# Optimization experiments

Measured on AMD Instinct MI355X. Metric: run time of the kernel, lower is better.

Reference implementation:

```python
import jax, jax.numpy as jnp
import numpy as np

B, S, H = 32, 256, 128
K, C, DSUB, O = 8, 4096, 16, 6  # PQ subspaces, ncentroids=4096, subvector dim, bits/symbol


def setup_inputs() -> dict:
    key = jax.random.key(0)
    ks = jax.random.split(key, 8)
    return {
        "z": jax.random.normal(ks[0], (B, S, 3), jnp.float32),
        "W1": jax.random.normal(ks[1], (3, H), jnp.float32) * 0.3,
        "b1": jax.random.normal(ks[2], (H,), jnp.float32) * 0.1,
        "W2": jax.random.normal(ks[3], (H, H), jnp.float32) * 0.1,
        "b2": jax.random.normal(ks[4], (H,), jnp.float32) * 0.1,
        "centroids": jax.random.normal(ks[5], (K, C, DSUB), jnp.float32),
        "W3": jax.random.normal(ks[6], (H, O), jnp.float32) * 0.1,
        "b3": jax.random.normal(ks[7], (O,), jnp.float32) * 0.1,
    }


def reference(z, W1, b1, W2, b2, centroids, W3, b3):
    # Small demapper MLP (layers 1-2, exact dense math)
    h1 = jax.nn.relu(z @ W1 + b1)            # [B,S,H]
    h2 = jax.nn.relu(h1 @ W2 + b2)           # [B,S,H] == layer3in
    N = B * S
    x = h2.reshape(N, K, DSUB)               # split rows into K PQ subvectors
    # Encode: nearest centroid per subspace (||x-c||^2 argmin; ||x||^2 is constant per row)
    dots = jnp.einsum("nkd,kcd->nkc", x, centroids)      # [N,K,C]
    c_norm = jnp.sum(centroids * centroids, axis=-1)      # [K,C]
    codes = jnp.argmin(c_norm[None, :, :] - 2.0 * dots, axis=-1)  # [N,K] int
    # LUT: precomputed centroid @ W3 per subspace
    W3r = W3.reshape(K, DSUB, O)
    lut = jnp.einsum("kcd,kdo->kco", centroids, W3r)      # [K,C,O]
    # Approximate matmul: sum of LUT entries selected by codes
    approx = jnp.sum(lut[jnp.arange(K)[None, :], codes], axis=1)  # [N,O]
    llr = (approx + b3).reshape(B, S * O)                 # [B, n]
    return llr
```

## Files before the change

### kernel.cpp

```cpp
#include <hip/hip_runtime.h>
#include <stdint.h>

#define NROWS 8192
#define HDIM  128
#define KSUB  8
#define NC    4096
#define DSUB  16
#define OUTD  6

#define FB_TAU 4e-3f
#define DOTSCALE (-2.0f / 4096.0f)

typedef _Float16 f16x8 __attribute__((ext_vector_type(8)));
typedef float    f32x4 __attribute__((ext_vector_type(4)));

#define XK_OFF 0u
#define CN_OFF 4194304u
#define B1_OFF 4325376u
#define PK_OFF 6422528u
#define M2_OFF 7471104u
#define CO_OFF B1_OFF

__global__ __launch_bounds__(256) void bprep_kernel(
    const float* __restrict__ ce, f16x8* __restrict__ B1)
{
    const int e = blockIdx.x * 256 + threadIdx.x;
    const int k    = e >> 14;
    const int tile = (e >> 6) & 255;
    const int lane = e & 63;
    const int col  = lane & 15;
    const int quad = lane >> 4;
    const int dims = (quad & 1) * 8;
    const int part = quad >> 1;
    const int n = tile * 16 + col;
    const float* cp = &ce[((size_t)k * NC + n) * DSUB + dims];
    f16x8 hi, lo;
    #pragma unroll
    for (int j = 0; j < 8; ++j) {
        const float s = cp[j] * 16.0f;
        const _Float16 h = (_Float16)s;
        hi[j] = h;
        lo[j] = (_Float16)(s - (float)h);
    }
    B1[e] = part ? lo : hi;
}

__global__ __launch_bounds__(256) void mlp_kernel(
    const float* __restrict__ z, const float* __restrict__ W1, const float* __restrict__ b1,
    const float* __restrict__ W2, const float* __restrict__ b2,
    const float* __restrict__ centroids,
    float* __restrict__ xk, float* __restrict__ cnorm)
{
    __shared__ float h1s[32 * HDIM];
    __shared__ float w2s[HDIM * HDIM];
    const int t = threadIdx.x;
    const int row0 = blockIdx.x * 32;

    if (blockIdx.x < (KSUB * NC) / 256) {
        const int g = blockIdx.x * 256 + t;
        const float4* cp = (const float4*)&centroids[(size_t)g * DSUB];
        float nn = 0.f;
        #pragma unroll
        for (int q = 0; q < 4; ++q) {
            const float4 v = cp[q];
            nn = fmaf(v.x, v.x, nn); nn = fmaf(v.y, v.y, nn);
            nn = fmaf(v.z, v.z, nn); nn = fmaf(v.w, v.w, nn);
        }
        cnorm[g] = nn;
    }

    {
        const float4* g4 = (const float4*)W2;
        float4* s4 = (float4*)w2s;
        #pragma unroll
        for (int q = 0; q < 16; ++q) s4[t + q * 256] = g4[t + q * 256];
    }

    #pragma unroll
    for (int e = 0; e < 16; ++e) {
        const int idx = e * 256 + t;
        const int r = idx >> 7, j = idx & 127;
        const int n = row0 + r;
        float acc = b1[j];
        acc = fmaf(z[n * 3 + 0], W1[0 * HDIM + j], acc);
        acc = fmaf(z[n * 3 + 1], W1[1 * HDIM + j], acc);
        acc = fmaf(z[n * 3 + 2], W1[2 * HDIM + j], acc);
        h1s[idx] = fmaxf(acc, 0.f);
    }
    __syncthreads();

    const int c4 = (t & 31) * 4;
    const int r4 = (t >> 5) * 4;
    float acc[4][4];
    #pragma unroll
    for (int a = 0; a < 4; ++a)
        #pragma unroll
        for (int b = 0; b < 4; ++b) acc[a][b] = 0.f;

    for (int k4 = 0; k4 < HDIM; k4 += 4) {
        float hh[4][4], ww[4][4];
        #pragma unroll
        for (int q = 0; q < 4; ++q) {
            const float4 v = *(const float4*)&h1s[(r4 + q) * HDIM + k4];
            hh[q][0] = v.x; hh[q][1] = v.y; hh[q][2] = v.z; hh[q][3] = v.w;
        }
        #pragma unroll
        for (int p = 0; p < 4; ++p) {
            const float4 v = *(const float4*)&w2s[(k4 + p) * HDIM + c4];
            ww[p][0] = v.x; ww[p][1] = v.y; ww[p][2] = v.z; ww[p][3] = v.w;
        }
        #pragma unroll
        for (int q = 0; q < 4; ++q)
            #pragma unroll
            for (int p = 0; p < 4; ++p) {
                acc[q][0] = fmaf(hh[q][p], ww[p][0], acc[q][0]);
                acc[q][1] = fmaf(hh[q][p], ww[p][1], acc[q][1]);
                acc[q][2] = fmaf(hh[q][p], ww[p][2], acc[q][2]);
                acc[q][3] = fmaf(hh[q][p], ww[p][3], acc[q][3]);
            }
    }

    const float4 bb = *(const float4*)&b2[c4];
    const int kk = c4 >> 4;
    const int dd = c4 & 15;
    #pragma unroll
    for (int q = 0; q < 4; ++q) {
        float4 o;
        o.x = fmaxf(acc[q][0] + bb.x, 0.f);
        o.y = fmaxf(acc[q][1] + bb.y, 0.f);
        o.z = fmaxf(acc[q][2] + bb.z, 0.f);
        o.w = fmaxf(acc[q][3] + bb.w, 0.f);
        *(float4*)&xk[((size_t)kk * NROWS + (row0 + r4 + q)) * DSUB + dd] = o;
    }
}

__global__ __launch_bounds__(256, 4) void argmin_kernel(
    const float* __restrict__ xk, const f16x8* __restrict__ B1,
    const float* __restrict__ cnorm,
    unsigned long long* __restrict__ pk, float* __restrict__ m2s)
{
    const int t = threadIdx.x;
    const int lane = t & 63;
    const int wid  = t >> 6;
    const int k  = blockIdx.y;
    const int cz = blockIdx.z;
    const int rb = blockIdx.x * 4 + wid;
    const int col  = lane & 15;
    const int quad = lane >> 4;
    const int dims = (quad & 1) * 8;
    const int part = quad >> 1;
    const int ct0 = cz * 128;

    f16x8 A[2];
    #pragma unroll
    for (int g = 0; g < 2; ++g) {
        const int row = rb * 32 + g * 16 + col;
        const float* xp = &xk[((size_t)k * NROWS + row) * DSUB + dims];
        f16x8 hi, lo;
        #pragma unroll
        for (int j = 0; j < 8; ++j) {
            const float s = xp[j] * 256.0f;
            const _Float16 h = (_Float16)s;
            hi[j] = h;
            lo[j] = (_Float16)(s - (float)h);
        }
        A[g] = part ? lo : hi;
    }

    float m1[2][4], m2[2][4];
    int   idx[2][4];
    #pragma unroll
    for (int g = 0; g < 2; ++g)
        #pragma unroll
        for (int j = 0; j < 4; ++j) { m1[g][j] = 1e30f; m2[g][j] = 1e30f; idx[g][j] = 0; }

    const f16x8* bp = &B1[((size_t)k * 256 + ct0) * 64];
    const float* cnp = &cnorm[k * NC + ct0 * 16 + col];
    const int l2 = lane ^ 32;

    f16x8 cb1 = bp[lane], cb2 = bp[l2];
    float cnv = cnp[0];

    for (int tt = 0; tt < 128; ++tt) {
        const f16x8 b1 = cb1, b2 = cb2;
        const float nrm = cnv;
        if (tt + 1 < 128) {
            cb1 = bp[(tt + 1) * 64 + lane];
            cb2 = bp[(tt + 1) * 64 + l2];
            cnv = cnp[(tt + 1) * 16];
        }
        f32x4 z4 = {0.f, 0.f, 0.f, 0.f};
        f32x4 a0a = __builtin_amdgcn_mfma_f32_16x16x32_f16(A[0], b1, z4, 0, 0, 0);
        f32x4 a0b = __builtin_amdgcn_mfma_f32_16x16x32_f16(A[0], b2, z4, 0, 0, 0);
        f32x4 a1a = __builtin_amdgcn_mfma_f32_16x16x32_f16(A[1], b1, z4, 0, 0, 0);
        f32x4 a1b = __builtin_amdgcn_mfma_f32_16x16x32_f16(A[1], b2, z4, 0, 0, 0);
        const int c = (ct0 + tt) * 16 + col;
        #pragma unroll
        for (int j = 0; j < 4; ++j) {
            {
                const float s = fmaf(a0a[j] + a0b[j], DOTSCALE, nrm);
                const bool lt = s < m1[0][j];
                m2[0][j] = __builtin_amdgcn_fmed3f(s, m1[0][j], m2[0][j]);
                idx[0][j] = lt ? c : idx[0][j];
                m1[0][j] = fminf(s, m1[0][j]);
            }
            {
                const float s = fmaf(a1a[j] + a1b[j], DOTSCALE, nrm);
                const bool lt = s < m1[1][j];
                m2[1][j] = __builtin_amdgcn_fmed3f(s, m1[1][j], m2[1][j]);
                idx[1][j] = lt ? c : idx[1][j];
                m1[1][j] = fminf(s, m1[1][j]);
            }
        }
    }

    #pragma unroll
    for (int off = 1; off < 16; off <<= 1) {
        #pragma unroll
        for (int g = 0; g < 2; ++g)
            #pragma unroll
            for (int j = 0; j < 4; ++j) {
                const float om1 = __shfl_xor(m1[g][j], off, 64);
                const float om2 = __shfl_xor(m2[g][j], off, 64);
                const int  oidx = __shfl_xor(idx[g][j], off, 64);
                const bool better = (om1 < m1[g][j]) ||
                                    (om1 == m1[g][j] && oidx < idx[g][j]);
                m2[g][j] = fminf(fminf(m2[g][j], om2), fmaxf(m1[g][j], om1));
                m1[g][j] = better ? om1 : m1[g][j];
                idx[g][j] = better ? oidx : idx[g][j];
            }
    }

    if (col == 0) {
        #pragma unroll
        for (int g = 0; g < 2; ++g)
            #pragma unroll
            for (int j = 0; j < 4; ++j) {
                const int row = rb * 32 + g * 16 + quad * 4 + j;
                unsigned u = __float_as_uint(m1[g][j]);
                u = (u & 0x80000000u) ? ~u : (u | 0x80000000u);
                pk [((size_t)cz * NROWS + row) * KSUB + k] =
                    ((unsigned long long)u << 32) | (unsigned)idx[g][j];
                m2s[((size_t)cz * NROWS + row) * KSUB + k] = m2[g][j];
            }
    }
}

__global__ __launch_bounds__(256) void fallback_kernel(
    const float* __restrict__ xk, const float* __restrict__ ce,
    const float* __restrict__ cnorm, const unsigned long long* __restrict__ pk,
    const float* __restrict__ m2s, int* __restrict__ codes)
{
    const int wg = blockIdx.x * 4 + (threadIdx.x >> 6);
    const int lane = threadIdx.x & 63;

    const unsigned long long a = pk[wg];
    const unsigned long long b = pk[(size_t)NROWS * KSUB + wg];
    const unsigned long long w = a < b ? a : b;
    const unsigned long long l = a < b ? b : a;
    const unsigned uw = (unsigned)(w >> 32), ul = (unsigned)(l >> 32);
    const float m1  = __uint_as_float((uw & 0x80000000u) ? (uw ^ 0x80000000u) : ~uw);
    const float m1l = __uint_as_float((ul & 0x80000000u) ? (ul ^ 0x80000000u) : ~ul);
    const float m2 = fminf(fminf(m2s[wg], m2s[(size_t)NROWS * KSUB + wg]), m1l);

    if (m2 - m1 >= FB_TAU) {
        if (lane == 0) codes[wg] = (int)(w & 0xFFFFFFFFull);
        return;
    }

    const int row = wg >> 3, k = wg & 7;
    float xr[DSUB];
    {
        const float* xp = &xk[((size_t)k * NROWS + row) * DSUB];
        #pragma unroll
        for (int q = 0; q < DSUB; q += 4) {
            const float4 v = *(const float4*)&xp[q];
            xr[q + 0] = -2.f * v.x; xr[q + 1] = -2.f * v.y;
            xr[q + 2] = -2.f * v.z; xr[q + 3] = -2.f * v.w;
        }
    }
    float bm = 1e30f; int bi = NC;
    for (int c = lane; c < NC; c += 64) {
        const float* cp = &ce[((size_t)k * NC + c) * DSUB];
        float s = cnorm[k * NC + c];
        #pragma unroll
        for (int d = 0; d < DSUB; ++d) s = fmaf(xr[d], cp[d], s);
        if (s < bm) { bm = s; bi = c; }
    }
    #pragma unroll
    for (int off = 1; off < 64; off <<= 1) {
        const float om = __shfl_xor(bm, off, 64);
        const int  oi = __shfl_xor(bi, off, 64);
        const bool better = (om < bm) || (om == bm && oi < bi);
        bm = better ? om : bm;
        bi = better ? oi : bi;
    }
    if (lane == 0) codes[wg] = bi;
}

__global__ __launch_bounds__(256) void out_kernel(
    const float* __restrict__ centroids, const float* __restrict__ W3,
    const float* __restrict__ b3, const int* __restrict__ codes,
    float* __restrict__ out)
{
    const int gid = blockIdx.x * 256 + threadIdx.x;
    const int n = gid / OUTD;
    const int o = gid - n * OUTD;
    float acc = b3[o];
    #pragma unroll
    for (int k = 0; k < KSUB; ++k) {
        const int code = codes[n * KSUB + k];
        const float* cp = &centroids[((size_t)k * NC + code) * DSUB];
        const float* wp = &W3[(k * DSUB) * OUTD + o];
        #pragma unroll
        for (int d = 0; d < DSUB; ++d)
            acc = fmaf(cp[d], wp[d * OUTD], acc);
    }
    out[gid] = acc;
}

extern "C" void kernel_launch(void* const* d_in, const int* in_sizes, int n_in,
                              void* d_out, int out_size, void* d_ws, size_t ws_size,
                              hipStream_t stream)
{
    const float* z  = (const float*)d_in[0];
    const float* W1 = (const float*)d_in[1];
    const float* b1 = (const float*)d_in[2];
    const float* W2 = (const float*)d_in[3];
    const float* b2 = (const float*)d_in[4];
    const float* ce = (const float*)d_in[5];
    const float* W3 = (const float*)d_in[6];
    const float* b3 = (const float*)d_in[7];

    char* ws = (char*)d_ws;
    float* xk     = (float*)(ws + XK_OFF);
    float* cnorm  = (float*)(ws + CN_OFF);
    f16x8* B1     = (f16x8*)(ws + B1_OFF);
    unsigned long long* pk = (unsigned long long*)(ws + PK_OFF);
    float* m2s    = (float*)(ws + M2_OFF);
    int*   codes  = (int*)  (ws + CO_OFF);

    hipLaunchKernelGGL(bprep_kernel, dim3(512), dim3(256), 0, stream, ce, B1);
    hipLaunchKernelGGL(mlp_kernel, dim3(NROWS / 32), dim3(256), 0, stream,
                       z, W1, b1, W2, b2, ce, xk, cnorm);
    hipLaunchKernelGGL(argmin_kernel, dim3(64, 8, 2), dim3(256), 0, stream,
                       xk, B1, cnorm, pk, m2s);
    hipLaunchKernelGGL(fallback_kernel, dim3(NROWS * KSUB / 4), dim3(256), 0, stream,
                       xk, ce, cnorm, pk, m2s, codes);
    hipLaunchKernelGGL(out_kernel, dim3((NROWS * OUTD) / 256), dim3(256), 0, stream,
                       ce, W3, b3, codes, (float*)d_out);
}
```

Baseline: 194.7 us.

## Fuse prep kernels, stage centroids in LDS, split argmin 4-way, merge fallback with output

Folds the centroid split-prep into the MLP kernel and merges the fallback and output kernels into one finish kernel that compacts the rows needing exact fallback into a worklist. Five launches become three. The argmin now splits centroids four ways, stages centroid tiles in shared memory, chains the hi/lo MFMAs into one accumulator, and packs the margin to the second-best as fp16 into the pk word, which removes the separate m2s buffer. The goals are less launch overhead, better grid parallelism and fewer global passes. In exchange the fp16 margin loses precision, the code field is narrowed to 16 bits, and the new __syncthreads add overhead in the argmin loop.

```diff
diff --git a/kernel.cpp b/kernel.cpp
--- a/kernel.cpp
+++ b/kernel.cpp
@@ -1,4 +1,5 @@
 #include <hip/hip_runtime.h>
+#include <hip/hip_fp16.h>
 #include <stdint.h>
 
 #define NROWS 8192
@@ -18,47 +19,46 @@
 #define CN_OFF 4194304u
 #define B1_OFF 4325376u
 #define PK_OFF 6422528u
-#define M2_OFF 7471104u
-#define CO_OFF B1_OFF
-
-__global__ __launch_bounds__(256) void bprep_kernel(
-    const float* __restrict__ ce, f16x8* __restrict__ B1)
-{
-    const int e = blockIdx.x * 256 + threadIdx.x;
-    const int k    = e >> 14;
-    const int tile = (e >> 6) & 255;
-    const int lane = e & 63;
-    const int col  = lane & 15;
-    const int quad = lane >> 4;
-    const int dims = (quad & 1) * 8;
-    const int part = quad >> 1;
-    const int n = tile * 16 + col;
-    const float* cp = &ce[((size_t)k * NC + n) * DSUB + dims];
-    f16x8 hi, lo;
-    #pragma unroll
-    for (int j = 0; j < 8; ++j) {
-        const float s = cp[j] * 16.0f;
-        const _Float16 h = (_Float16)s;
-        hi[j] = h;
-        lo[j] = (_Float16)(s - (float)h);
-    }
-    B1[e] = part ? lo : hi;
-}
-
-__global__ __launch_bounds__(256) void mlp_kernel(
+
+__global__ __launch_bounds__(256) void prep_kernel(
     const float* __restrict__ z, const float* __restrict__ W1, const float* __restrict__ b1,
     const float* __restrict__ W2, const float* __restrict__ b2,
-    const float* __restrict__ centroids,
-    float* __restrict__ xk, float* __restrict__ cnorm)
+    const float* __restrict__ ce,
+    float* __restrict__ xk, float* __restrict__ cnorm, f16x8* __restrict__ B1S)
 {
     __shared__ float h1s[32 * HDIM];
     __shared__ float w2s[HDIM * HDIM];
     const int t = threadIdx.x;
-    const int row0 = blockIdx.x * 32;
-
-    if (blockIdx.x < (KSUB * NC) / 256) {
-        const int g = blockIdx.x * 256 + t;
-        const float4* cp = (const float4*)&centroids[(size_t)g * DSUB];
+
+    if (blockIdx.x < 512) {
+        const int e = blockIdx.x * 256 + t;
+        const int k    = e >> 14;
+        const int tile = (e >> 6) & 255;
+        const int lane = e & 63;
+        const int col  = lane & 15;
+        const int quad = lane >> 4;
+        const int dims = (quad & 1) * 8;
+        const int part = quad >> 1;
+        const int n = tile * 16 + col;
+        const float* cp = &ce[((size_t)k * NC + n) * DSUB + dims];
+        f16x8 hi, lo;
+        #pragma unroll
+        for (int j = 0; j < 8; ++j) {
+            const float s = cp[j] * 16.0f;
+            const _Float16 h = (_Float16)s;
+            hi[j] = h;
+            lo[j] = (_Float16)(s - (float)h);
+        }
+        B1S[e] = part ? lo : hi;
+        return;
+    }
+
+    const int bx = blockIdx.x - 512;
+    const int row0 = bx * 32;
+
+    if (bx < (KSUB * NC) / 256) {
+        const int g = bx * 256 + t;
+        const float4* cp = (const float4*)&ce[(size_t)g * DSUB];
         float nn = 0.f;
         #pragma unroll
         for (int q = 0; q < 4; ++q) {
@@ -135,10 +135,10 @@
 }
 
 __global__ __launch_bounds__(256, 4) void argmin_kernel(
-    const float* __restrict__ xk, const f16x8* __restrict__ B1,
-    const float* __restrict__ cnorm,
-    unsigned long long* __restrict__ pk, float* __restrict__ m2s)
+    const float* __restrict__ xk, const f16x8* __restrict__ B1S,
+    const float* __restrict__ cnorm, unsigned long long* __restrict__ pk)
 {
+    __shared__ f16x8 cs[16 * 64];
     const int t = threadIdx.x;
     const int lane = t & 63;
     const int wid  = t >> 6;
@@ -149,7 +149,6 @@
     const int quad = lane >> 4;
     const int dims = (quad & 1) * 8;
     const int part = quad >> 1;
-    const int ct0 = cz * 128;
 
     f16x8 A[2];
     #pragma unroll
@@ -174,42 +173,48 @@
         #pragma unroll
         for (int j = 0; j < 4; ++j) { m1[g][j] = 1e30f; m2[g][j] = 1e30f; idx[g][j] = 0; }
 
-    const f16x8* bp = &B1[((size_t)k * 256 + ct0) * 64];
-    const float* cnp = &cnorm[k * NC + ct0 * 16 + col];
-    const int l2 = lane ^ 32;
-
-    f16x8 cb1 = bp[lane], cb2 = bp[l2];
-    float cnv = cnp[0];
-
-    for (int tt = 0; tt < 128; ++tt) {
-        const f16x8 b1 = cb1, b2 = cb2;
-        const float nrm = cnv;
-        if (tt + 1 < 128) {
-            cb1 = bp[(tt + 1) * 64 + lane];
-            cb2 = bp[(tt + 1) * 64 + l2];
-            cnv = cnp[(tt + 1) * 16];
-        }
-        f32x4 z4 = {0.f, 0.f, 0.f, 0.f};
-        f32x4 a0a = __builtin_amdgcn_mfma_f32_16x16x32_f16(A[0], b1, z4, 0, 0, 0);
-        f32x4 a0b = __builtin_amdgcn_mfma_f32_16x16x32_f16(A[0], b2, z4, 0, 0, 0);
-        f32x4 a1a = __builtin_amdgcn_mfma_f32_16x16x32_f16(A[1], b1, z4, 0, 0, 0);
-        f32x4 a1b = __builtin_amdgcn_mfma_f32_16x16x32_f16(A[1], b2, z4, 0, 0, 0);
-        const int c = (ct0 + tt) * 16 + col;
-        #pragma unroll
-        for (int j = 0; j < 4; ++j) {
-            {
-                const float s = fmaf(a0a[j] + a0b[j], DOTSCALE, nrm);
-                const bool lt = s < m1[0][j];
-                m2[0][j] = __builtin_amdgcn_fmed3f(s, m1[0][j], m2[0][j]);
-                idx[0][j] = lt ? c : idx[0][j];
-                m1[0][j] = fminf(s, m1[0][j]);
-            }
-            {
-                const float s = fmaf(a1a[j] + a1b[j], DOTSCALE, nrm);
-                const bool lt = s < m1[1][j];
-                m2[1][j] = __builtin_amdgcn_fmed3f(s, m1[1][j], m2[1][j]);
-                idx[1][j] = lt ? c : idx[1][j];
-                m1[1][j] = fminf(s, m1[1][j]);
+    const f16x8* gp  = &B1S[((size_t)k * 256 + cz * 64) * 64];
+    const float* cnp = &cnorm[k * NC + cz * 64 * 16 + col];
+
+    for (int ch = 0; ch < 4; ++ch) {
+        __syncthreads();
+        {
+            const uint4* g4 = (const uint4*)(gp + (size_t)ch * 1024);
+            uint4* s4 = (uint4*)cs;
+            #pragma unroll
+            for (int q = 0; q < 4; ++q) s4[t + q * 256] = g4[t + q * 256];
+        }
+        float nr[16];
+        #pragma unroll
+        for (int tt = 0; tt < 16; ++tt) nr[tt] = cnp[(ch * 16 + tt) * 16];
+        __syncthreads();
+
+        #pragma unroll
+        for (int tt = 0; tt < 16; ++tt) {
+            const f16x8 b1 = cs[tt * 64 + lane];
+            const f16x8 b2 = cs[tt * 64 + (lane ^ 32)];
+            const f32x4 zz = {0.f, 0.f, 0.f, 0.f};
+            f32x4 p0 = __builtin_amdgcn_mfma_f32_16x16x32_f16(A[0], b1, zz, 0, 0, 0);
+            p0       = __builtin_amdgcn_mfma_f32_16x16x32_f16(A[0], b2, p0, 0, 0, 0);
+            f32x4 p1 = __builtin_amdgcn_mfma_f32_16x16x32_f16(A[1], b1, zz, 0, 0, 0);
+            p1       = __builtin_amdgcn_mfma_f32_16x16x32_f16(A[1], b2, p1, 0, 0, 0);
+            const int c = ((cz * 64 + ch * 16 + tt) << 4) + col;
+            #pragma unroll
+            for (int j = 0; j < 4; ++j) {
+                {
+                    const float s = fmaf(p0[j], DOTSCALE, nr[tt]);
+                    const bool lt = s < m1[0][j];
+                    m2[0][j] = __builtin_amdgcn_fmed3f(s, m1[0][j], m2[0][j]);
+                    idx[0][j] = lt ? c : idx[0][j];
+                    m1[0][j] = fminf(s, m1[0][j]);
+                }
+                {
+                    const float s = fmaf(p1[j], DOTSCALE, nr[tt]);
+                    const bool lt = s < m1[1][j];
+                    m2[1][j] = __builtin_amdgcn_fmed3f(s, m1[1][j], m2[1][j]);
+                    idx[1][j] = lt ? c : idx[1][j];
+                    m1[1][j] = fminf(s, m1[1][j]);
+                }
             }
         }
     }
@@ -239,84 +244,112 @@
                 const int row = rb * 32 + g * 16 + quad * 4 + j;
                 unsigned u = __float_as_uint(m1[g][j]);
                 u = (u & 0x80000000u) ? ~u : (u | 0x80000000u);
-                pk [((size_t)cz * NROWS + row) * KSUB + k] =
-                    ((unsigned long long)u << 32) | (unsigned)idx[g][j];
-                m2s[((size_t)cz * NROWS + row) * KSUB + k] = m2[g][j];
+                const unsigned short dh =
+                    __half_as_ushort(__float2half(m2[g][j] - m1[g][j]));
+                pk[((size_t)cz * NROWS + row) * KSUB + k] =
+                    ((unsigned long long)u << 32) |
+                    ((unsigned)dh << 16) | (unsigned)idx[g][j];
             }
     }
 }
 
-__global__ __launch_bounds__(256) void fallback_kernel(
+__global__ __launch_bounds__(256) void finish_kernel(
     const float* __restrict__ xk, const float* __restrict__ ce,
     const float* __restrict__ cnorm, const unsigned long long* __restrict__ pk,
-    const float* __restrict__ m2s, int* __restrict__ codes)
-{
-    const int wg = blockIdx.x * 4 + (threadIdx.x >> 6);
-    const int lane = threadIdx.x & 63;
-
-    const unsigned long long a = pk[wg];
-    const unsigned long long b = pk[(size_t)NROWS * KSUB + wg];
-    const unsigned long long w = a < b ? a : b;
-    const unsigned long long l = a < b ? b : a;
-    const unsigned uw = (unsigned)(w >> 32), ul = (unsigned)(l >> 32);
-    const float m1  = __uint_as_float((uw & 0x80000000u) ? (uw ^ 0x80000000u) : ~uw);
-    const float m1l = __uint_as_float((ul & 0x80000000u) ? (ul ^ 0x80000000u) : ~ul);
-    const float m2 = fminf(fminf(m2s[wg], m2s[(size_t)NROWS * KSUB + wg]), m1l);
-
-    if (m2 - m1 >= FB_TAU) {
-        if (lane == 0) codes[wg] = (int)(w & 0xFFFFFFFFull);
-        return;
-    }
-
-    const int row = wg >> 3, k = wg & 7;
-    float xr[DSUB];
-    {
-        const float* xp = &xk[((size_t)k * NROWS + row) * DSUB];
-        #pragma unroll
-        for (int q = 0; q < DSUB; q += 4) {
-            const float4 v = *(const float4*)&xp[q];
-            xr[q + 0] = -2.f * v.x; xr[q + 1] = -2.f * v.y;
-            xr[q + 2] = -2.f * v.z; xr[q + 3] = -2.f * v.w;
-        }
-    }
-    float bm = 1e30f; int bi = NC;
-    for (int c = lane; c < NC; c += 64) {
-        const float* cp = &ce[((size_t)k * NC + c) * DSUB];
-        float s = cnorm[k * NC + c];
-        #pragma unroll
-        for (int d = 0; d < DSUB; ++d) s = fmaf(xr[d], cp[d], s);
-        if (s < bm) { bm = s; bi = c; }
-    }
-    #pragma unroll
-    for (int off = 1; off < 64; off <<= 1) {
-        const float om = __shfl_xor(bm, off, 64);
-        const int  oi = __shfl_xor(bi, off, 64);
-        const bool better = (om < bm) || (om == bm && oi < bi);
-        bm = better ? om : bm;
-        bi = better ? oi : bi;
-    }
-    if (lane == 0) codes[wg] = bi;
-}
-
-__global__ __launch_bounds__(256) void out_kernel(
-    const float* __restrict__ centroids, const float* __restrict__ W3,
-    const float* __restrict__ b3, const int* __restrict__ codes,
+    const float* __restrict__ W3, const float* __restrict__ b3,
     float* __restrict__ out)
 {
-    const int gid = blockIdx.x * 256 + threadIdx.x;
-    const int n = gid / OUTD;
-    const int o = gid - n * OUTD;
-    float acc = b3[o];
-    #pragma unroll
-    for (int k = 0; k < KSUB; ++k) {
-        const int code = codes[n * KSUB + k];
-        const float* cp = &centroids[((size_t)k * NC + code) * DSUB];
-        const float* wp = &W3[(k * DSUB) * OUTD + o];
-        #pragma unroll
-        for (int d = 0; d < DSUB; ++d)
-            acc = fmaf(cp[d], wp[d * OUTD], acc);
-    }
-    out[gid] = acc;
+    __shared__ int codes_s[256];
+    __shared__ int wl_s[256];
+    __shared__ int wcnt;
+    const int t = threadIdx.x;
+    const int row0 = blockIdx.x * 32;
+    if (t == 0) wcnt = 0;
+    __syncthreads();
+
+    {
+        const int row = row0 + (t >> 3);
+        const int k = t & 7;
+        unsigned long long p[4];
+        #pragma unroll
+        for (int s = 0; s < 4; ++s)
+            p[s] = pk[((size_t)s * NROWS + row) * KSUB + k];
+        unsigned long long w = p[0];
+        #pragma unroll
+        for (int s = 1; s < 4; ++s) w = p[s] < w ? p[s] : w;
+        const unsigned uw = (unsigned)(w >> 32);
+        const float m1w = __uint_as_float((uw & 0x80000000u) ? (uw ^ 0x80000000u) : ~uw);
+        float m2g = m1w + (float)__ushort_as_half((unsigned short)((unsigned)w >> 16));
+        #pragma unroll
+        for (int s = 0; s < 4; ++s) {
+            if (p[s] != w) {
+                const unsigned us = (unsigned)(p[s] >> 32);
+                m2g = fminf(m2g, __uint_as_float(
+                    (us & 0x80000000u) ? (us ^ 0x80000000u) : ~us));
+            }
+        }
+        codes_s[t] = (int)(w & 0xFFFFull);
+        if (m2g - m1w < FB_TAU) {
+            const int slot = atomicAdd(&wcnt, 1);
+            wl_s[slot] = t;
+        }
+    }
+    __syncthreads();
+
+    {
+        const int lane = t & 63;
+        const int wid = t >> 6;
+        const int nitems = wcnt;
+        for (int i = wid; i < nitems; i += 4) {
+            const int wg = wl_s[i];
+            const int row = row0 + (wg >> 3), k = wg & 7;
+            float xr[DSUB];
+            {
+                const float* xp = &xk[((size_t)k * NROWS + row) * DSUB];
+                #pragma unroll
+                for (int q = 0; q < DSUB; q += 4) {
+                    const float4 v = *(const float4*)&xp[q];
+                    xr[q + 0] = -2.f * v.x; xr[q + 1] = -2.f * v.y;
+                    xr[q + 2] = -2.f * v.z; xr[q + 3] = -2.f * v.w;
+                }
+            }
+            float bm = 1e30f; int bi = NC;
+            for (int c = lane; c < NC; c += 64) {
+                const float* cp = &ce[((size_t)k * NC + c) * DSUB];
+                float s = cnorm[k * NC + c];
+                #pragma unroll
+                for (int d = 0; d < DSUB; ++d) s = fmaf(xr[d], cp[d], s);
+                if (s < bm) { bm = s; bi = c; }
+            }
+            #pragma unroll
+            for (int off = 1; off < 64; off <<= 1) {
+                const float om = __shfl_xor(bm, off, 64);
+                const int  oi = __shfl_xor(bi, off, 64);
+                const bool better = (om < bm) || (om == bm && oi < bi);
+                bm = better ? om : bm;
+                bi = better ? oi : bi;
+            }
+            if (lane == 0) codes_s[wg] = bi;
+        }
+    }
+    __syncthreads();
+
+    if (t < 32 * OUTD) {
+        const int nl = t / OUTD;
+        const int o = t - nl * OUTD;
+        const int n = row0 + nl;
+        float acc = b3[o];
+        #pragma unroll
+        for (int k = 0; k < KSUB; ++k) {
+            const int code = codes_s[nl * KSUB + k];
+            const float* cp = &ce[((size_t)k * NC + code) * DSUB];
+            const float* wp = &W3[(k * DSUB) * OUTD + o];
+            #pragma unroll
+            for (int d = 0; d < DSUB; ++d)
+                acc = fmaf(cp[d], wp[d * OUTD], acc);
+        }
+        out[n * OUTD + o] = acc;
+    }
 }
 
 extern "C" void kernel_launch(void* const* d_in, const int* in_sizes, int n_in,
@@ -333,20 +366,15 @@
     const float* b3 = (const float*)d_in[7];
 
     char* ws = (char*)d_ws;
-    float* xk     = (float*)(ws + XK_OFF);
-    float* cnorm  = (float*)(ws + CN_OFF);
-    f16x8* B1     = (f16x8*)(ws + B1_OFF);
+    float* xk    = (float*)(ws + XK_OFF);
+    float* cnorm = (float*)(ws + CN_OFF);
+    f16x8* B1S   = (f16x8*)(ws + B1_OFF);
     unsigned long long* pk = (unsigned long long*)(ws + PK_OFF);
-    float* m2s    = (float*)(ws + M2_OFF);
-    int*   codes  = (int*)  (ws + CO_OFF);
-
-    hipLaunchKernelGGL(bprep_kernel, dim3(512), dim3(256), 0, stream, ce, B1);
-    hipLaunchKernelGGL(mlp_kernel, dim3(NROWS / 32), dim3(256), 0, stream,
-                       z, W1, b1, W2, b2, ce, xk, cnorm);
-    hipLaunchKernelGGL(argmin_kernel, dim3(64, 8, 2), dim3(256), 0, stream,
-                       xk, B1, cnorm, pk, m2s);
-    hipLaunchKernelGGL(fallback_kernel, dim3(NROWS * KSUB / 4), dim3(256), 0, stream,
-                       xk, ce, cnorm, pk, m2s, codes);
-    hipLaunchKernelGGL(out_kernel, dim3((NROWS * OUTD) / 256), dim3(256), 0, stream,
-                       ce, W3, b3, codes, (float*)d_out);
+
+    hipLaunchKernelGGL(prep_kernel, dim3(768), dim3(256), 0, stream,
+                       z, W1, b1, W2, b2, ce, xk, cnorm, B1S);
+    hipLaunchKernelGGL(argmin_kernel, dim3(64, 8, 4), dim3(256), 0, stream,
+                       xk, B1S, cnorm, pk);
+    hipLaunchKernelGGL(finish_kernel, dim3(256), dim3(256), 0, stream,
+                       xk, ce, cnorm, pk, W3, b3, (float*)d_out);
 }
```

Measured after the change: 221.6 us. 1.14x slower.
